# Performance work log

Measured on AMD Instinct MI355X. Metric: run time of the kernel, lower is better.

## Reference

```python
import jax, jax.numpy as jnp
import numpy as np

B, C, H, W = 2, 64, 128, 128
KH = KW = 3
K = KH * KW
PAD = 1


def conv(x, w, b, pad):
    out = jax.lax.conv_general_dilated(
        x, w, window_strides=(1, 1), padding=[(pad, pad), (pad, pad)],
        dimension_numbers=("NCHW", "OIHW", "NCHW"))
    return out + b[None, :, None, None]


def leaky_relu(x, slope=0.2):
    return jnp.where(x >= 0, x, slope * x)


def deform_conv(img, offset, mask, w, b):
    # img: [B,C,Hi,Wi]; offset: [B,2K,H,W] (dy,dx interleaved per tap); mask: [B,K,H,W]
    Bb, Ci, Hi, Wi = img.shape
    Ho, Wo = offset.shape[2], offset.shape[3]
    off = offset.reshape(Bb, K, 2, Ho, Wo)
    dy, dx = off[:, :, 0], off[:, :, 1]
    ki, kj = jnp.meshgrid(jnp.arange(KH), jnp.arange(KW), indexing="ij")
    ki = ki.reshape(K).astype(img.dtype)
    kj = kj.reshape(K).astype(img.dtype)
    base_h = (jnp.arange(Ho) - PAD).astype(img.dtype)
    base_w = (jnp.arange(Wo) - PAD).astype(img.dtype)
    ys = base_h[None, None, :, None] + ki[None, :, None, None] + dy  # [B,K,Ho,Wo]
    xs = base_w[None, None, None, :] + kj[None, :, None, None] + dx

    y0 = jnp.floor(ys)
    x0 = jnp.floor(xs)
    ty = ys - y0
    tx = xs - x0
    y0i = y0.astype(jnp.int32)
    x0i = x0.astype(jnp.int32)
    flat = img.reshape(Bb, Ci, Hi * Wi)

    def corner(yi, xi, wgt):
        valid = (yi >= 0) & (yi < Hi) & (xi >= 0) & (xi < Wi)
        yc = jnp.clip(yi, 0, Hi - 1)
        xc = jnp.clip(xi, 0, Wi - 1)
        idx = (yc * Wi + xc).reshape(Bb, 1, -1)
        v = jnp.take_along_axis(flat, jnp.broadcast_to(idx, (Bb, Ci, idx.shape[-1])), axis=2)
        v = v.reshape(Bb, Ci, K, Ho, Wo)
        return v * (wgt * valid.astype(img.dtype))[:, None]

    samp = (corner(y0i, x0i, (1 - ty) * (1 - tx))
            + corner(y0i, x0i + 1, (1 - ty) * tx)
            + corner(y0i + 1, x0i, ty * (1 - tx))
            + corner(y0i + 1, x0i + 1, ty * tx))  # [B,C,K,Ho,Wo]
    out = jnp.einsum("ock,bckhw->bohw", w.reshape(w.shape[0], Ci, K), samp * mask[:, None])
    return out + b[None, :, None, None]


def setup_inputs() -> dict:
    key = jax.random.key(0)
    ks = jax.random.split(key, 8)
    s = 0.05  # keep predicted offsets in a realistic few-pixel range
    return {
        "x": jax.random.normal(ks[0], (B, C, H, W), jnp.float32),
        "y": jax.random.normal(ks[1], (B, C, H, W), jnp.float32),
        "w0": jax.random.normal(ks[2], (C, C, 1, 1), jnp.float32) * s,
        "b0": jnp.zeros((C,), jnp.float32),
        "w_om": jax.random.normal(ks[3], (3 * K, 2 * C, KH, KW), jnp.float32) * s,
        "b_om": jnp.zeros((3 * K,), jnp.float32),
        "w_dc": jax.random.normal(ks[4], (C, C, KH, KW), jnp.float32) * s,
        "b_dc": jnp.zeros((C,), jnp.float32),
        "w1": jax.random.normal(ks[5], (C, C, KH, KW), jnp.float32) * s,
        "b1": jnp.zeros((C,), jnp.float32),
        "w2": jax.random.normal(ks[6], (C, C, KH, KW), jnp.float32) * s,
        "b2": jnp.zeros((C,), jnp.float32),
    }


def reference(x, y, w0, b0, w_om, b_om, w_dc, b_dc, w1, b1, w2, b2):
    x0 = conv(x, w0, b0, pad=0)  # 1x1 projection
    om = conv(jnp.concatenate([x0, y], axis=1), w_om, b_om, pad=PAD)
    offset = om[:, : 2 * K]
    mask = 2.0 * jax.nn.sigmoid(om[:, 2 * K :])
    out = x0 + deform_conv(y, offset, mask, w_dc, b_dc)
    return conv(leaky_relu(conv(out, w1, b1, pad=PAD)), w2, b2, pad=PAD) + out
```

## Files before the change

### kernel.cpp

```cpp
#include <hip/hip_runtime.h>
#include <hip/hip_bf16.h>
#include <math.h>

#define BB 2
#define CCH 64
#define HH 128
#define WWD 128
#define HWv (HH*WWD)
#define KK 9
#define KSTEP 18
#define OMKS 36
#define TCOLS 34
#define CSTR 72
#define CSTR2 136
#define DROW 584

typedef __attribute__((ext_vector_type(8))) short bf16x8;
typedef __attribute__((ext_vector_type(4))) float f32x4;
typedef unsigned short u16;
typedef unsigned int u32;

__device__ inline u16 f2bf(float f) {
  __hip_bfloat16 h = __float2bfloat16(f);
  return *reinterpret_cast<u16*>(&h);
}
__device__ inline u32 f2bf2(float lo, float hi) {
  return ((u32)f2bf(hi) << 16) | (u32)f2bf(lo);
}
__device__ inline float bfLO(u32 v) { return __uint_as_float(v << 16); }
__device__ inline float bfHI(u32 v) { return __uint_as_float(v & 0xffff0000u); }
__device__ inline float bf2f(u16 v) { return __uint_as_float((u32)v << 16); }

__global__ __launch_bounds__(256) void pack_all_k(
    const float* __restrict__ w_dc, const float* __restrict__ w1,
    const float* __restrict__ w2, const float* __restrict__ w_om,
    const float* __restrict__ w0, u16* __restrict__ pk_dc,
    u16* __restrict__ pk_w1, u16* __restrict__ pk_w2,
    u16* __restrict__ pk_om, u16* __restrict__ pk_0) {
  int blk = blockIdx.x;
  int tid = threadIdx.x;
  if (blk < 432) {
    const float* w = blk < 144 ? w_dc : (blk < 288 ? w1 : w2);
    u16* dst = blk < 144 ? pk_dc : (blk < 288 ? pk_w1 : pk_w2);
    int idx = (blk % 144) * 256 + tid;
    int j = idx & 7, l = (idx >> 3) & 63;
    int s = (idx >> 9) % 18, q = idx / 9216;
    int co = q * 16 + (l & 15);
    int kp = s * 32 + (l >> 4) * 8 + j;
    dst[idx] = f2bf(w[(co * 64 + (kp & 63)) * 9 + (kp >> 6)]);
  } else if (blk < 576) {
    int idx = (blk - 432) * 256 + tid;
    int j = idx & 7, l = (idx >> 3) & 63;
    int s = (idx >> 9) % 36, q = idx / 18432;
    int co = q * 16 + (l & 15);
    int kp = s * 32 + (l >> 4) * 8 + j;
    pk_om[idx] = (co < 27)
        ? f2bf(w_om[(co * 128 + (kp & 127)) * 9 + (kp >> 7)]) : (u16)0;
  } else {
    int idx = (blk - 576) * 256 + tid;
    int j = idx & 7, l = (idx >> 3) & 63;
    int s = (idx >> 9) & 1, q = idx / 1024;
    int co = q * 16 + (l & 15);
    int k = s * 32 + (l >> 4) * 8 + j;
    pk_0[idx] = f2bf(w0[co * 64 + k]);
  }
}

__global__ __launch_bounds__(256) void conv1x1y_k(const float* __restrict__ x,
    const float* __restrict__ y, const u16* __restrict__ wpack,
    const float* __restrict__ b0, u16* __restrict__ x0bf,
    u16* __restrict__ yt) {
  #define S1ROW 72
  __shared__ __align__(16) float smem[64 * 65];
  u16* samp1 = (u16*)smem;
  int tid = threadIdx.x;
  int lane = tid & 63, q = tid >> 6;
  int pixbase = blockIdx.x * 64;
  int hwb = pixbase & (HWv - 1);
  int b = pixbase >> 14;

  {
    const float* src = y + (size_t)b * CCH * HWv;
    #pragma unroll
    for (int i = 0; i < 16; i++) {
      int ci = i * 4 + q;
      smem[ci * 65 + lane] = src[(size_t)ci * HWv + hwb + lane];
    }
    __syncthreads();
    u32* dst32 = (u32*)(yt + ((size_t)b * HWv + hwb) * 64);
    int lane2 = tid & 31, rr = tid >> 5;
    #pragma unroll
    for (int i = 0; i < 8; i++) {
      int row = i * 8 + rr;
      dst32[row * 32 + lane2] = f2bf2(smem[(2 * lane2) * 65 + row],
                                      smem[(2 * lane2 + 1) * 65 + row]);
    }
    __syncthreads();
  }

  {
    u16 tmp[16];
    #pragma unroll
    for (int i = 0; i < 16; i++) {
      int ci = q * 16 + i;
      tmp[i] = f2bf(x[((size_t)b * CCH + ci) * HWv + hwb + lane]);
    }
    #pragma unroll
    for (int i = 0; i < 2; i++)
      *(bf16x8*)(samp1 + lane * S1ROW + q * 16 + i * 8) = *(bf16x8*)(tmp + i * 8);
  }
  __syncthreads();
  f32x4 acc[4] = {{0,0,0,0},{0,0,0,0},{0,0,0,0},{0,0,0,0}};
  int g = lane >> 4;
  const bf16x8* bp = (const bf16x8*)wpack + (size_t)(q * 2) * 64 + lane;
  #pragma unroll
  for (int s = 0; s < 2; s++) {
    bf16x8 bf = bp[(size_t)s * 64];
    #pragma unroll
    for (int t = 0; t < 4; t++) {
      bf16x8 a = *(const bf16x8*)(samp1 + (t * 16 + (lane & 15)) * S1ROW + g * 8 + s * 32);
      acc[t] = __builtin_amdgcn_mfma_f32_16x16x32_bf16(a, bf, acc[t], 0, 0, 0);
    }
  }
  int co = q * 16 + (lane & 15);
  float bv = b0[co];
  u16* dst = x0bf + ((size_t)b * HWv + hwb + g * 4) * 64 + co;
  #pragma unroll
  for (int t = 0; t < 4; t++)
    #pragma unroll
    for (int r = 0; r < 4; r++)
      dst[(size_t)(t * 16 + r) * 64] = f2bf(acc[t][r] + bv);
}

__global__ __launch_bounds__(512) void omd_k(const u16* __restrict__ x0bf,
    const u16* __restrict__ yt, const u16* __restrict__ pk_om,
    const u16* __restrict__ pk_dc, const float* __restrict__ b_om,
    const float* __restrict__ b_dc, u16* __restrict__ ob) {
  __shared__ __align__(16) u16 A[18688];
  __shared__ __align__(16) int prm[288][8];
  __shared__ __align__(16) float omv[64 * 28];
  u32* A32 = (u32*)A;
  u32* dsamp32 = (u32*)A;
  u16* dsamp = A;
  int tid = threadIdx.x;
  int lane = tid & 63, q = tid >> 6;
  int blk = blockIdx.x;
  int wq = blk & 3, rp = (blk >> 2) & 63, b = blk >> 8;
  int h0 = rp * 2, wb = wq * 32;
  const u32* x0b32 = (const u32*)x0bf + (size_t)b * HWv * 32;
  const u32* yt32  = (const u32*)yt + (size_t)b * HWv * 32;

  {
    int lane2 = tid & 31, g16 = tid >> 5;
    int cofs = lane2 * 2;
    const u32* srcb = (lane2 < 16) ? (x0b32 + cofs) : (yt32 + cofs - 32);
    #pragma unroll
    for (int i = 0; i < 9; i++) {
      int u = g16 + 16 * i;
      if (u < 4 * TCOLS) {
        int r = u / TCOLS, c = u % TCOLS;
        int hh = h0 - 1 + r, ww = wb - 1 + c;
        uint2 v = {0u, 0u};
        if ((unsigned)hh < HH && (unsigned)ww < WWD)
          v = *(const uint2*)(srcb + (size_t)(hh * WWD + ww) * 32);
        *(uint2*)(A32 + u * (CSTR2 / 2) + cofs) = v;
      }
    }
  }
  __syncthreads();

  {
    int r = q & 1, cg = (q >> 1) & 1, cohalf = q >> 2;
    f32x4 acc = {0.f, 0.f, 0.f, 0.f};
    const bf16x8* bp = (const bf16x8*)pk_om + (size_t)(cohalf * OMKS) * 64 + lane;
    #pragma unroll
    for (int s = 0; s < OMKS; s++) {
      int kk = s >> 2;
      int addr = ((r + kk / 3) * TCOLS + cg * 16 + (lane & 15) + (kk % 3)) * CSTR2
                 + (s & 3) * 32 + (lane >> 4) * 8;
      bf16x8 a = *(const bf16x8*)(A + addr);
      acc = __builtin_amdgcn_mfma_f32_16x16x32_bf16(a, bp[(size_t)s * 64], acc, 0, 0, 0);
    }
    int co = cohalf * 16 + (lane & 15);
    if (co < 27) {
      float bv = b_om[co];
      int px = r * 32 + cg * 16 + (lane >> 4) * 4;
      #pragma unroll
      for (int j = 0; j < 4; j++)
        omv[(px + j) * 28 + co] = acc[j] + bv;
    }
  }
  __syncthreads();

  for (int h2 = 0; h2 < 2; h2++) {
    if (tid < 32 * KK) {
      int pl = tid / KK, k = tid % KK;
      const float* omp = omv + (h2 * 32 + pl) * 28;
      float dy = omp[2 * k], dx = omp[2 * k + 1];
      float mk = 2.f / (1.f + expf(-omp[18 + k]));
      float ys = (float)(h0 + h2 - 1 + k / 3) + dy;
      float xs = (float)(wb + pl - 1 + k % 3) + dx;
      float y0f = floorf(ys), x0f = floorf(xs);
      float ty = ys - y0f, tx = xs - x0f;
      int yi = (int)y0f, xi = (int)x0f;
      bool y0v = (unsigned)yi < HH, y1v = (unsigned)(yi + 1) < HH;
      bool x0v = (unsigned)xi < WWD, x1v = (unsigned)(xi + 1) < WWD;
      float w00 = (1.f - ty) * (1.f - tx) * mk * ((y0v && x0v) ? 1.f : 0.f);
      float w01 = (1.f - ty) * tx * mk * ((y0v && x1v) ? 1.f : 0.f);
      float w10 = ty * (1.f - tx) * mk * ((y1v && x0v) ? 1.f : 0.f);
      float w11 = ty * tx * mk * ((y1v && x1v) ? 1.f : 0.f);
      int* p = prm[tid];
      *(int4*)p = make_int4(min(max(yi, 0), HH - 1) * (WWD * 32),
                            min(max(yi + 1, 0), HH - 1) * (WWD * 32),
                            min(max(xi, 0), WWD - 1) * 32,
                            min(max(xi + 1, 0), WWD - 1) * 32);
      *(int4*)(p + 4) = make_int4(__float_as_int(w00), __float_as_int(w01),
                                  __float_as_int(w10), __float_as_int(w11));
    }
    __syncthreads();
    {
      int lane4 = tid & 15, g16 = tid >> 4;
      const u32* ytb = yt32 + lane4 * 2;
      #pragma unroll
      for (int i = 0; i < 9; i++) {
        int u = g16 + 32 * i;
        int k = u % 9, pix = u / 9;
        int4 pa = *(const int4*)prm[u];
        int4 pb = *(const int4*)(prm[u] + 4);
        uint2 v00 = *(const uint2*)(ytb + pa.x + pa.z);
        uint2 v01 = *(const uint2*)(ytb + pa.x + pa.w);
        uint2 v10 = *(const uint2*)(ytb + pa.y + pa.z);
        uint2 v11 = *(const uint2*)(ytb + pa.y + pa.w);
        float w00 = __int_as_float(pb.x), w01 = __int_as_float(pb.y);
        float w10 = __int_as_float(pb.z), w11 = __int_as_float(pb.w);
        float a0 = fmaf(bfLO(v00.x), w00, fmaf(bfLO(v01.x), w01,
                   fmaf(bfLO(v10.x), w10, bfLO(v11.x) * w11)));
        float a1 = fmaf(bfHI(v00.x), w00, fmaf(bfHI(v01.x), w01,
                   fmaf(bfHI(v10.x), w10, bfHI(v11.x) * w11)));
        float a2 = fmaf(bfLO(v00.y), w00, fmaf(bfLO(v01.y), w01,
                   fmaf(bfLO(v10.y), w10, bfLO(v11.y) * w11)));
        float a3 = fmaf(bfHI(v00.y), w00, fmaf(bfHI(v01.y), w01,
                   fmaf(bfHI(v10.y), w10, bfHI(v11.y) * w11)));
        uint2 o = {f2bf2(a0, a1), f2bf2(a2, a3)};
        *(uint2*)(dsamp32 + pix * (DROW / 2) + k * 32 + lane4 * 2) = o;
      }
    }
    __syncthreads();
    {
      int qq = q & 3, pxg = q >> 2;
      f32x4 acc = {0.f, 0.f, 0.f, 0.f};
      const u16* arow = dsamp + (pxg * 16 + (lane & 15)) * DROW + (lane >> 4) * 8;
      const bf16x8* bp = (const bf16x8*)pk_dc + (size_t)(qq * KSTEP) * 64 + lane;
      #pragma unroll
      for (int s = 0; s < KSTEP; s++) {
        bf16x8 a = *(const bf16x8*)(arow + s * 32);
        acc = __builtin_amdgcn_mfma_f32_16x16x32_bf16(a, bp[(size_t)s * 64], acc, 0, 0, 0);
      }
      int co = qq * 16 + (lane & 15);
      int px = pxg * 16 + (lane >> 4) * 4;
      float bv = b_dc[co];
      size_t obase = ((size_t)b * HWv + (h0 + h2) * WWD + wb + px) * 64 + co;
      #pragma unroll
      for (int j = 0; j < 4; j++)
        ob[obase + (size_t)j * 64] =
            f2bf(acc[j] + bv + bf2f(x0bf[obase + (size_t)j * 64]));
    }
    __syncthreads();
  }
}

template <int MODE>
__global__ __launch_bounds__(512) void rconv_k(const u16* __restrict__ in,
    const u16* __restrict__ res, const u16* __restrict__ wpack,
    const float* __restrict__ bias, void* __restrict__ outp) {
  __shared__ __align__(16) u16 samp[4 * TCOLS * CSTR];
  u32* samp32 = (u32*)samp;
  int tid = threadIdx.x;
  int blk = blockIdx.x;
  int wq = blk & 3, rp = (blk >> 2) & 63, b = blk >> 8;
  int h0 = rp * 2, wb = wq * 32;

  {
    int lane4 = tid & 15, g16 = tid >> 4;
    const u32* inb = (const u32*)in + (size_t)b * HWv * 32 + lane4 * 2;
    #pragma unroll
    for (int i = 0; i < 5; i++) {
      int u = g16 + 32 * i;
      if (u < 4 * TCOLS) {
        int r = u / TCOLS, c = u % TCOLS;
        int hh = h0 - 1 + r, ww = wb - 1 + c;
        uint2 v = {0u, 0u};
        if ((unsigned)hh < HH && (unsigned)ww < WWD)
          v = *(const uint2*)(inb + (size_t)(hh * WWD + ww) * 32);
        *(uint2*)(samp32 + u * (CSTR / 2) + lane4 * 2) = v;
      }
    }
  }
  __syncthreads();

  int lane = tid & 63, q = tid >> 6;
  int r = q & 1, cg = (q >> 1) & 1, copair = q >> 2;
  f32x4 acc[2] = {{0,0,0,0},{0,0,0,0}};
  const bf16x8* bp = (const bf16x8*)wpack + (size_t)(copair * 2 * KSTEP) * 64 + lane;
  #pragma unroll
  for (int s = 0; s < KSTEP; s++) {
    int kk = s >> 1;
    int addr = ((r + kk / 3) * TCOLS + cg * 16 + (lane & 15) + (kk % 3)) * CSTR
               + (s & 1) * 32 + (lane >> 4) * 8;
    bf16x8 a = *(const bf16x8*)(samp + addr);
    acc[0] = __builtin_amdgcn_mfma_f32_16x16x32_bf16(a, bp[(size_t)s * 64], acc[0], 0, 0, 0);
    acc[1] = __builtin_amdgcn_mfma_f32_16x16x32_bf16(a, bp[(size_t)(KSTEP + s) * 64], acc[1], 0, 0, 0);
  }

  int pxc = cg * 16 + (lane >> 4) * 4;
  int hwp = (h0 + r) * WWD + wb + pxc;
  if (MODE == 1) {
    u16* outb = (u16*)outp;
    #pragma unroll
    for (int t = 0; t < 2; t++) {
      int co = copair * 32 + t * 16 + (lane & 15);
      float bv = bias[co];
      size_t obase = ((size_t)b * HWv + hwp) * 64 + co;
      #pragma unroll
      for (int j = 0; j < 4; j++) {
        float v = acc[t][j] + bv;
        outb[obase + (size_t)j * 64] = f2bf(v >= 0.f ? v : 0.2f * v);
      }
    }
  } else {
    float* outf = (float*)outp;
    float* ot = (float*)samp;
    __syncthreads();
    #pragma unroll
    for (int t = 0; t < 2; t++) {
      int co = copair * 32 + t * 16 + (lane & 15);
      float bv = bias[co];
      size_t rbase = ((size_t)b * HWv + hwp) * 64 + co;
      #pragma unroll
      for (int j = 0; j < 4; j++)
        ot[co * 72 + r * 36 + pxc + j] = acc[t][j] + bv + bf2f(res[rbase + (size_t)j * 64]);
    }
    __syncthreads();
    int co = tid >> 3, seg = tid & 7;
    int r2 = seg >> 2, c8 = (seg & 3) * 8;
    const float4* src4 = (const float4*)(ot + co * 72 + r2 * 36 + c8);
    float4 v0 = src4[0], v1 = src4[1];
    float* dst = outf + ((size_t)b * CCH + co) * HWv + (h0 + r2) * WWD + wb + c8;
    *(float4*)dst = v0;
    *(float4*)(dst + 4) = v1;
  }
}

extern "C" void kernel_launch(void* const* d_in, const int* in_sizes, int n_in,
                              void* d_out, int out_size, void* d_ws, size_t ws_size,
                              hipStream_t stream) {
  const float* x    = (const float*)d_in[0];
  const float* y    = (const float*)d_in[1];
  const float* w0   = (const float*)d_in[2];
  const float* b0   = (const float*)d_in[3];
  const float* w_om = (const float*)d_in[4];
  const float* b_om = (const float*)d_in[5];
  const float* w_dc = (const float*)d_in[6];
  const float* b_dc = (const float*)d_in[7];
  const float* w1   = (const float*)d_in[8];
  const float* b1   = (const float*)d_in[9];
  const float* w2   = (const float*)d_in[10];
  const float* b2   = (const float*)d_in[11];
  float* out = (float*)d_out;

  const size_t NFULL = (size_t)BB * CCH * HWv;
  const size_t NPACK = 4 * KSTEP * 64 * 8;
  const size_t NPACKOM = 2 * OMKS * 64 * 8;
  u16* x0bf = (u16*)d_ws;
  u16* ob   = x0bf + NFULL;
  u16* z1   = ob + NFULL;
  u16* yt   = z1;
  u16* pk_dc = z1 + NFULL;
  u16* pk_w1 = pk_dc + NPACK;
  u16* pk_w2 = pk_w1 + NPACK;
  u16* pk_om = pk_w2 + NPACK;
  u16* pk_0  = pk_om + NPACKOM;

  const int NB = (int)((size_t)BB * HWv / 64);

  pack_all_k<<<592, 256, 0, stream>>>(w_dc, w1, w2, w_om, w0,
                                      pk_dc, pk_w1, pk_w2, pk_om, pk_0);
  conv1x1y_k<<<NB, 256, 0, stream>>>(x, y, pk_0, b0, x0bf, yt);
  omd_k<<<NB, 512, 0, stream>>>(x0bf, yt, pk_om, pk_dc, b_om, b_dc, ob);
  rconv_k<1><<<NB, 512, 0, stream>>>(ob, nullptr, pk_w1, b1, z1);
  rconv_k<2><<<NB, 512, 0, stream>>>(z1, ob, pk_w2, b2, out);
}
```

Before: 63.86 us.

## Fuse the two trailing 3x3 convs into one kernel with halo recompute

Merges the two residual 3x3 convolution launches into a single kernel. Each block stages a 6x36 halo tile of the deform output, computes the leaky-ReLU intermediate for a 4x34 region in LDS, then applies the second conv and the residual add from shared memory. This removes the global write and read of the bf16 intermediate and one kernel launch. In exchange it recomputes halo rows of the first conv, about 2x the work of that conv, and uses more LDS per block, which may lower occupancy.

```diff
diff --git a/kernel.cpp b/kernel.cpp
--- a/kernel.cpp
+++ b/kernel.cpp
@@ -269,86 +269,107 @@
   }
 }
 
-template <int MODE>
-__global__ __launch_bounds__(512) void rconv_k(const u16* __restrict__ in,
-    const u16* __restrict__ res, const u16* __restrict__ wpack,
-    const float* __restrict__ bias, void* __restrict__ outp) {
-  __shared__ __align__(16) u16 samp[4 * TCOLS * CSTR];
-  u32* samp32 = (u32*)samp;
+__global__ __launch_bounds__(512) void rconv12_k(const u16* __restrict__ ob,
+    const u16* __restrict__ pk_w1, const u16* __restrict__ pk_w2,
+    const float* __restrict__ b1, const float* __restrict__ b2,
+    float* __restrict__ outp) {
+  #define R2COLS 36
+  __shared__ __align__(16) u16 stage[6 * R2COLS * CSTR];
+  __shared__ __align__(16) u16 zlds[144 * CSTR];
+  u32* stage32 = (u32*)stage;
   int tid = threadIdx.x;
+  int lane = tid & 63, q = tid >> 6;
   int blk = blockIdx.x;
   int wq = blk & 3, rp = (blk >> 2) & 63, b = blk >> 8;
   int h0 = rp * 2, wb = wq * 32;
 
   {
     int lane4 = tid & 15, g16 = tid >> 4;
-    const u32* inb = (const u32*)in + (size_t)b * HWv * 32 + lane4 * 2;
-    #pragma unroll
-    for (int i = 0; i < 5; i++) {
+    const u32* inb = (const u32*)ob + (size_t)b * HWv * 32 + lane4 * 2;
+    #pragma unroll
+    for (int i = 0; i < 7; i++) {
       int u = g16 + 32 * i;
-      if (u < 4 * TCOLS) {
-        int r = u / TCOLS, c = u % TCOLS;
-        int hh = h0 - 1 + r, ww = wb - 1 + c;
+      if (u < 6 * R2COLS) {
+        int r = u / R2COLS, c = u % R2COLS;
+        int hh = h0 - 2 + r, ww = wb - 2 + c;
         uint2 v = {0u, 0u};
         if ((unsigned)hh < HH && (unsigned)ww < WWD)
           v = *(const uint2*)(inb + (size_t)(hh * WWD + ww) * 32);
-        *(uint2*)(samp32 + u * (CSTR / 2) + lane4 * 2) = v;
-      }
-    }
-  }
-  __syncthreads();
-
-  int lane = tid & 63, q = tid >> 6;
+        *(uint2*)(stage32 + u * (CSTR / 2) + lane4 * 2) = v;
+      }
+    }
+  }
+  __syncthreads();
+
+  #pragma unroll
+  for (int t = 0; t < 5; t++) {
+    int task = q + 8 * t;
+    if (task < 36) {
+      int g = task >> 2, coq = task & 3;
+      int p = g * 16 + (lane & 15);
+      if (p > 135) p = 135;
+      int r1 = p / 34, c1 = p % 34;
+      f32x4 acc = {0.f, 0.f, 0.f, 0.f};
+      const bf16x8* bp = (const bf16x8*)pk_w1 + (size_t)(coq * KSTEP) * 64 + lane;
+      #pragma unroll
+      for (int s = 0; s < KSTEP; s++) {
+        int kk = s >> 1;
+        int addr = ((r1 + kk / 3) * R2COLS + c1 + kk % 3) * CSTR
+                   + (s & 1) * 32 + (lane >> 4) * 8;
+        bf16x8 a = *(const bf16x8*)(stage + addr);
+        acc = __builtin_amdgcn_mfma_f32_16x16x32_bf16(a, bp[(size_t)s * 64], acc, 0, 0, 0);
+      }
+      int co = coq * 16 + (lane & 15);
+      float bv = b1[co];
+      int prow = g * 16 + (lane >> 4) * 4;
+      #pragma unroll
+      for (int j = 0; j < 4; j++) {
+        int pp = prow + j;
+        int rr = pp / 34, cc = pp % 34;
+        bool inimg = ((unsigned)(h0 - 1 + rr) < HH) && ((unsigned)(wb - 1 + cc) < WWD);
+        float v = acc[j] + bv;
+        v = v >= 0.f ? v : 0.2f * v;
+        zlds[pp * CSTR + co] = inimg ? f2bf(v) : (u16)0;
+      }
+    }
+  }
+  __syncthreads();
+
   int r = q & 1, cg = (q >> 1) & 1, copair = q >> 2;
-  f32x4 acc[2] = {{0,0,0,0},{0,0,0,0}};
-  const bf16x8* bp = (const bf16x8*)wpack + (size_t)(copair * 2 * KSTEP) * 64 + lane;
+  f32x4 acc2[2] = {{0,0,0,0},{0,0,0,0}};
+  const bf16x8* bp2 = (const bf16x8*)pk_w2 + (size_t)(copair * 2 * KSTEP) * 64 + lane;
   #pragma unroll
   for (int s = 0; s < KSTEP; s++) {
     int kk = s >> 1;
-    int addr = ((r + kk / 3) * TCOLS + cg * 16 + (lane & 15) + (kk % 3)) * CSTR
-               + (s & 1) * 32 + (lane >> 4) * 8;
-    bf16x8 a = *(const bf16x8*)(samp + addr);
-    acc[0] = __builtin_amdgcn_mfma_f32_16x16x32_bf16(a, bp[(size_t)s * 64], acc[0], 0, 0, 0);
-    acc[1] = __builtin_amdgcn_mfma_f32_16x16x32_bf16(a, bp[(size_t)(KSTEP + s) * 64], acc[1], 0, 0, 0);
-  }
-
+    int p = (r + kk / 3) * 34 + cg * 16 + (lane & 15) + (kk % 3);
+    int addr = p * CSTR + (s & 1) * 32 + (lane >> 4) * 8;
+    bf16x8 a = *(const bf16x8*)(zlds + addr);
+    acc2[0] = __builtin_amdgcn_mfma_f32_16x16x32_bf16(a, bp2[(size_t)s * 64], acc2[0], 0, 0, 0);
+    acc2[1] = __builtin_amdgcn_mfma_f32_16x16x32_bf16(a, bp2[(size_t)(KSTEP + s) * 64], acc2[1], 0, 0, 0);
+  }
+  __syncthreads();
+
+  float* ot = (float*)zlds;
   int pxc = cg * 16 + (lane >> 4) * 4;
-  int hwp = (h0 + r) * WWD + wb + pxc;
-  if (MODE == 1) {
-    u16* outb = (u16*)outp;
-    #pragma unroll
-    for (int t = 0; t < 2; t++) {
-      int co = copair * 32 + t * 16 + (lane & 15);
-      float bv = bias[co];
-      size_t obase = ((size_t)b * HWv + hwp) * 64 + co;
-      #pragma unroll
-      for (int j = 0; j < 4; j++) {
-        float v = acc[t][j] + bv;
-        outb[obase + (size_t)j * 64] = f2bf(v >= 0.f ? v : 0.2f * v);
-      }
-    }
-  } else {
-    float* outf = (float*)outp;
-    float* ot = (float*)samp;
-    __syncthreads();
-    #pragma unroll
-    for (int t = 0; t < 2; t++) {
-      int co = copair * 32 + t * 16 + (lane & 15);
-      float bv = bias[co];
-      size_t rbase = ((size_t)b * HWv + hwp) * 64 + co;
-      #pragma unroll
-      for (int j = 0; j < 4; j++)
-        ot[co * 72 + r * 36 + pxc + j] = acc[t][j] + bv + bf2f(res[rbase + (size_t)j * 64]);
-    }
-    __syncthreads();
-    int co = tid >> 3, seg = tid & 7;
-    int r2 = seg >> 2, c8 = (seg & 3) * 8;
-    const float4* src4 = (const float4*)(ot + co * 72 + r2 * 36 + c8);
-    float4 v0 = src4[0], v1 = src4[1];
-    float* dst = outf + ((size_t)b * CCH + co) * HWv + (h0 + r2) * WWD + wb + c8;
-    *(float4*)dst = v0;
-    *(float4*)(dst + 4) = v1;
-  }
+  #pragma unroll
+  for (int t = 0; t < 2; t++) {
+    int co = copair * 32 + t * 16 + (lane & 15);
+    float bv = b2[co];
+    #pragma unroll
+    for (int j = 0; j < 4; j++) {
+      int c = pxc + j;
+      u16 resv = stage[((r + 2) * R2COLS + c + 2) * CSTR + co];
+      ot[co * 72 + r * 36 + c] = acc2[t][j] + bv + bf2f(resv);
+    }
+  }
+  __syncthreads();
+  int co = tid >> 3, seg = tid & 7;
+  int r2 = seg >> 2, c8 = (seg & 3) * 8;
+  const float4* src4 = (const float4*)(ot + co * 72 + r2 * 36 + c8);
+  float4 v0 = src4[0], v1 = src4[1];
+  float* dst = outp + ((size_t)b * CCH + co) * HWv + (h0 + r2) * WWD + wb + c8;
+  *(float4*)dst = v0;
+  *(float4*)(dst + 4) = v1;
 }
 
 extern "C" void kernel_launch(void* const* d_in, const int* in_sizes, int n_in,
@@ -373,9 +394,8 @@
   const size_t NPACKOM = 2 * OMKS * 64 * 8;
   u16* x0bf = (u16*)d_ws;
   u16* ob   = x0bf + NFULL;
-  u16* z1   = ob + NFULL;
-  u16* yt   = z1;
-  u16* pk_dc = z1 + NFULL;
+  u16* yt   = ob + NFULL;
+  u16* pk_dc = yt + NFULL;
   u16* pk_w1 = pk_dc + NPACK;
   u16* pk_w2 = pk_w1 + NPACK;
   u16* pk_om = pk_w2 + NPACK;
@@ -387,6 +407,5 @@
                                       pk_dc, pk_w1, pk_w2, pk_om, pk_0);
   conv1x1y_k<<<NB, 256, 0, stream>>>(x, y, pk_0, b0, x0bf, yt);
   omd_k<<<NB, 512, 0, stream>>>(x0bf, yt, pk_om, pk_dc, b_om, b_dc, ob);
-  rconv_k<1><<<NB, 512, 0, stream>>>(ob, nullptr, pk_w1, b1, z1);
-  rconv_k<2><<<NB, 512, 0, stream>>>(z1, ob, pk_w2, b2, out);
-}
+  rconv12_k<<<NB, 512, 0, stream>>>(ob, pk_w1, pk_w2, b1, b2, out);
+}
```

Result: faster. 60.43 us (median of 2 runs) (-5.4%).
